# Kernel optimization log

Measured on AMD Instinct MI355X. Metric: run time of the kernel, lower is better.

Reference implementation:

```python
import jax, jax.numpy as jnp
from jax import lax
import numpy as np

DIM = 2048
KSZ = 4
BATCH = 4
SEQ = 4096


def setup_inputs() -> dict:
    key = jax.random.key(0)
    k1, k2 = jax.random.split(key)
    x = jax.random.normal(k1, (BATCH, SEQ, DIM), dtype=jnp.float32)
    weight = jax.random.normal(k2, (DIM, 1, KSZ), dtype=jnp.float32) * 0.02
    bias = jnp.zeros((DIM,), dtype=jnp.float32)
    return {"x": x, "weight": weight, "bias": bias}


def reference(x, weight, bias):
    # x: (B, S, D); weight: (D, 1, K) torch layout; bias: (D,)
    K = weight.shape[-1]
    # causal left-pad along sequence
    xp = jnp.pad(x, ((0, 0), (K - 1, 0), (0, 0)))
    # depthwise conv: NWC input, WIO kernel with in-per-group=1, groups=D
    w = jnp.transpose(weight, (2, 1, 0))  # (K, 1, D)
    y = lax.conv_general_dilated(
        xp, w,
        window_strides=(1,),
        padding='VALID',
        dimension_numbers=('NWC', 'WIO', 'NWC'),
        feature_group_count=x.shape[-1],
    )
    return y + bias  # (B, S, D)
```

## Files before the change

kernel.cpp:

```cpp
#include <hip/hip_runtime.h>

#define BB 4
#define SS 4096
#define DD 2048
#define KK 4
#define D4 (DD / 4)
#define CHUNK 16
#define NCH (SS / CHUNK)
#define NLD (CHUNK + 3)

typedef float f32x4 __attribute__((ext_vector_type(4)));


__device__ __forceinline__ float4 conv4(const float4 bv,
                                        const float4 wr0, const float4 wr1,
                                        const float4 wr2, const float4 wr3,
                                        const float4 xm3, const float4 xm2,
                                        const float4 xm1, const float4 xc) {
  float4 r;
  r.x = bv.x + wr0.x * xm3.x + wr0.y * xm2.x + wr0.z * xm1.x + wr0.w * xc.x;
  r.y = bv.y + wr1.x * xm3.y + wr1.y * xm2.y + wr1.z * xm1.y + wr1.w * xc.y;
  r.z = bv.z + wr2.x * xm3.z + wr2.y * xm2.z + wr2.z * xm1.z + wr2.w * xc.z;
  r.w = bv.w + wr3.x * xm3.w + wr3.y * xm2.w + wr3.z * xm1.w + wr3.w * xc.w;
  return r;
}

__device__ __forceinline__ void nt_store4(float4* p, const float4 v) {
  f32x4 tmp;
  tmp.x = v.x; tmp.y = v.y; tmp.z = v.z; tmp.w = v.w;
  __builtin_nontemporal_store(tmp, (f32x4*)p);
}

__global__ __launch_bounds__(256, 4) void shortconv_kernel(
    const float4* __restrict__ x,
    const float4* __restrict__ w4,
    const float4* __restrict__ bias4,
    float4* __restrict__ y)
{
    const int t    = blockIdx.x * 256 + threadIdx.x;
    const int d4   = t & (D4 - 1);
    const int rest = t >> 9;
    const int ch   = rest & (NCH - 1);
    const int b    = rest >> 8;

    const int s0 = ch * CHUNK;
    const size_t base = ((size_t)b * SS + (size_t)s0) * D4 + (size_t)d4;

    float4 a[NLD];
    if (ch == 0) {
        a[0] = make_float4(0.f, 0.f, 0.f, 0.f);
        a[1] = a[0];
        a[2] = a[0];
    } else {
        a[0] = x[base - 3 * (size_t)D4];
        a[1] = x[base - 2 * (size_t)D4];
        a[2] = x[base - 1 * (size_t)D4];
    }
#pragma unroll
    for (int i = 0; i < CHUNK; ++i) {
        a[i + 3] = x[base + (size_t)i * D4];
    }

    const float4 wr0 = w4[4 * d4 + 0];
    const float4 wr1 = w4[4 * d4 + 1];
    const float4 wr2 = w4[4 * d4 + 2];
    const float4 wr3 = w4[4 * d4 + 3];
    const float4 bv  = bias4[d4];

    __builtin_amdgcn_sched_barrier(0);

#pragma unroll
    for (int i = 0; i < CHUNK; ++i) {
        const float4 r = conv4(bv, wr0, wr1, wr2, wr3,
                               a[i], a[i + 1], a[i + 2], a[i + 3]);
        nt_store4(&y[base + (size_t)i * D4], r);
    }
}

extern "C" void kernel_launch(void* const* d_in, const int* in_sizes, int n_in,
                              void* d_out, int out_size, void* d_ws, size_t ws_size,
                              hipStream_t stream) {
    const float* x    = (const float*)d_in[0];
    const float* w    = (const float*)d_in[1];
    const float* bias = (const float*)d_in[2];
    float* out        = (float*)d_out;

    const int total_threads = BB * NCH * D4;
    const int block = 256;
    const int grid  = total_threads / block;

    shortconv_kernel<<<grid, block, 0, stream>>>(
        (const float4*)x, (const float4*)w, (const float4*)bias, (float4*)out);
}
```

Before: 238.5 us.

## Stage input rows through LDS via direct global-to-LDS loads with smaller chunks

Replaces per-thread register loads of the sequence window with global_load_lds transfers into a shared tile per block. Each block now handles half the channels for an 8-row chunk instead of 16, and reads a rolling window from LDS. The aim is more memory parallelism without register pressure. In exchange the halo re-read overhead rises and a block-wide barrier is added.

```diff
diff --git a/kernel.cpp b/kernel.cpp
--- a/kernel.cpp
+++ b/kernel.cpp
@@ -5,9 +5,10 @@
 #define DD 2048
 #define KK 4
 #define D4 (DD / 4)
-#define CHUNK 16
+#define CHUNK 8
 #define NCH (SS / CHUNK)
-#define NLD (CHUNK + 3)
+#define ROWS (CHUNK + 3)
+#define HALF 256
 
 typedef float f32x4 __attribute__((ext_vector_type(4)));
 
@@ -31,49 +32,66 @@
   __builtin_nontemporal_store(tmp, (f32x4*)p);
 }
 
-__global__ __launch_bounds__(256, 4) void shortconv_kernel(
+#define GLD_LDS(gp, lp)                                                       \
+  __builtin_amdgcn_global_load_lds(                                          \
+      (const __attribute__((address_space(1))) void*)(gp),                   \
+      (__attribute__((address_space(3))) void*)(lp), 16, 0, 0)
+
+__global__ __launch_bounds__(256) void shortconv_kernel(
     const float4* __restrict__ x,
     const float4* __restrict__ w4,
     const float4* __restrict__ bias4,
     float4* __restrict__ y)
 {
-    const int t    = blockIdx.x * 256 + threadIdx.x;
-    const int d4   = t & (D4 - 1);
-    const int rest = t >> 9;
-    const int ch   = rest & (NCH - 1);
-    const int b    = rest >> 8;
+    __shared__ float4 sx[ROWS][HALF];
+
+    const int blk  = blockIdx.x;
+    const int half = blk & 1;
+    const int ch   = (blk >> 1) & (NCH - 1);
+    const int b    = blk >> 10;
+
+    const int ld4  = threadIdx.x;
+    const int g_d4 = half * HALF + ld4;
+    const int wave = threadIdx.x >> 6;
 
     const int s0 = ch * CHUNK;
-    const size_t base = ((size_t)b * SS + (size_t)s0) * D4 + (size_t)d4;
+    const size_t base = ((size_t)b * SS + (size_t)s0) * D4 + (size_t)g_d4;
 
-    float4 a[NLD];
-    if (ch == 0) {
-        a[0] = make_float4(0.f, 0.f, 0.f, 0.f);
-        a[1] = a[0];
-        a[2] = a[0];
+    const float4 wr0 = w4[4 * g_d4 + 0];
+    const float4 wr1 = w4[4 * g_d4 + 1];
+    const float4 wr2 = w4[4 * g_d4 + 2];
+    const float4 wr3 = w4[4 * g_d4 + 3];
+    const float4 bv  = bias4[g_d4];
+
+    if (ch != 0) {
+#pragma unroll
+        for (int r = 0; r < ROWS; ++r) {
+            GLD_LDS(x + base + (size_t)(r - 3) * D4, &sx[r][wave << 6]);
+        }
     } else {
-        a[0] = x[base - 3 * (size_t)D4];
-        a[1] = x[base - 2 * (size_t)D4];
-        a[2] = x[base - 1 * (size_t)D4];
+        const float4 z = make_float4(0.f, 0.f, 0.f, 0.f);
+        sx[0][ld4] = z;
+        sx[1][ld4] = z;
+        sx[2][ld4] = z;
+#pragma unroll
+        for (int r = 3; r < ROWS; ++r) {
+            GLD_LDS(x + base + (size_t)(r - 3) * D4, &sx[r][wave << 6]);
+        }
     }
+
+    __syncthreads();
+
+    float4 x0 = sx[0][ld4];
+    float4 x1 = sx[1][ld4];
+    float4 x2 = sx[2][ld4];
 #pragma unroll
     for (int i = 0; i < CHUNK; ++i) {
-        a[i + 3] = x[base + (size_t)i * D4];
-    }
-
-    const float4 wr0 = w4[4 * d4 + 0];
-    const float4 wr1 = w4[4 * d4 + 1];
-    const float4 wr2 = w4[4 * d4 + 2];
-    const float4 wr3 = w4[4 * d4 + 3];
-    const float4 bv  = bias4[d4];
-
-    __builtin_amdgcn_sched_barrier(0);
-
-#pragma unroll
-    for (int i = 0; i < CHUNK; ++i) {
-        const float4 r = conv4(bv, wr0, wr1, wr2, wr3,
-                               a[i], a[i + 1], a[i + 2], a[i + 3]);
+        const float4 x3 = sx[i + 3][ld4];
+        const float4 r = conv4(bv, wr0, wr1, wr2, wr3, x0, x1, x2, x3);
         nt_store4(&y[base + (size_t)i * D4], r);
+        x0 = x1;
+        x1 = x2;
+        x2 = x3;
     }
 }
 
@@ -85,9 +103,8 @@
     const float* bias = (const float*)d_in[2];
     float* out        = (float*)d_out;
 
-    const int total_threads = BB * NCH * D4;
+    const int grid  = BB * NCH * 2;
     const int block = 256;
-    const int grid  = total_threads / block;
 
     shortconv_kernel<<<grid, block, 0, stream>>>(
         (const float4*)x, (const float4*)w, (const float4*)bias, (float4*)out);
```

Result: faster. 231.7 us (-2.9%).
